# Performance work log

Measured on AMD Instinct MI355X. Metric: run time of the kernel, lower is better.

## Reference

```python
import jax, jax.numpy as jnp
import numpy as np

K = 10
EPS = 1e-5

def leaky(x):
    return jnp.where(x >= 0, x, 0.2 * x)

def graph_feature(x, k):
    # x: (B, C, N) -> edge features (B, 2C, N, k), standard DGCNN get_graph_feature
    B, C, N = x.shape
    xx = jnp.sum(x * x, axis=1)                      # (B, N)
    inner = jnp.einsum('bcn,bcm->bnm', x, x)          # (B, N, N)
    pair = 2.0 * inner - xx[:, :, None] - xx[:, None, :]  # -||xi - xj||^2
    _, idx = jax.lax.top_k(pair, k)                   # (B, N, k)
    xt = jnp.transpose(x, (0, 2, 1))                  # (B, N, C)
    nbr = xt[jnp.arange(B)[:, None, None], idx]       # (B, N, k, C) gather
    ctr = jnp.broadcast_to(xt[:, :, None, :], nbr.shape)
    feat = jnp.concatenate([nbr - ctr, ctr], axis=-1)  # (B, N, k, 2C)
    return jnp.transpose(feat, (0, 3, 1, 2))          # (B, 2C, N, k)

def edge_block(x, W, k):
    # gather -> 1x1 conv (edge MLP) -> leaky relu -> max over neighbors
    e = graph_feature(x, k)                           # (B, 2C, N, k)
    h = leaky(jnp.einsum('oc,bcnk->bonk', W, e))      # (B, O, N, k)
    return jnp.max(h, axis=-1)                        # (B, O, N)

def bn(x, g, b, m, v):
    # inference batchnorm over channel axis 1; x: (B, C, ...) 
    shape = (1, -1) + (1,) * (x.ndim - 2)
    return (x - m.reshape(shape)) * (g.reshape(shape) * jax.lax.rsqrt(v.reshape(shape) + EPS)) + b.reshape(shape)

def setup_inputs() -> dict:
    key = jax.random.key(0)
    ks = jax.random.split(key, 20)
    s = lambda i, shape, scale: (jax.random.normal(ks[i], shape, jnp.float32) * scale)
    inp = {
        'input': jax.random.normal(ks[0], (759, 220, 3), jnp.float32),
        'W1': s(1, (32, 6), 0.4),
        'W2': s(2, (32, 64), 0.15),
        'W3': s(3, (64, 64), 0.15),
        'W4': s(4, (128, 128), 0.1),
        'W5': s(5, (512, 256), 0.08),
        'g5': 1.0 + s(6, (512,), 0.05), 'b5': s(7, (512,), 0.05),
        'm5': s(8, (512,), 0.05), 'v5': 1.0 + 0.1 * jax.random.uniform(ks[9], (512,), jnp.float32),
        'Wl1': s(10, (1024, 1024), 0.03),
        'g6': 1.0 + s(11, (1024,), 0.05), 'b6': s(12, (1024,), 0.05),
        'm6': s(13, (1024,), 0.05), 'v6': 1.0 + 0.1 * jax.random.uniform(ks[14], (1024,), jnp.float32),
        'Wl2': s(15, (380, 1024), 0.03),
        'bl2': s(16, (380,), 0.02),
    }
    return inp

def reference(input, W1, W2, W3, W4, W5, g5, b5, m5, v5, Wl1, g6, b6, m6, v6, Wl2, bl2):
    x = jnp.transpose(input.reshape(-1, 220, 3), (0, 2, 1))  # (B, 3, N)
    x1 = edge_block(x, W1, K)    # (B, 32, N)
    x2 = edge_block(x1, W2, K)   # (B, 32, N)
    x3 = edge_block(x2, W3, K)   # (B, 64, N)
    x4 = edge_block(x3, W4, K)   # (B, 128, N)
    xc = jnp.concatenate([x1, x2, x3, x4], axis=1)           # (B, 256, N)
    h = leaky(bn(jnp.einsum('oc,bcn->bon', W5, xc), g5, b5, m5, v5))  # (B, 512, N)
    p = jnp.concatenate([jnp.max(h, axis=-1), jnp.mean(h, axis=-1)], axis=1)  # (B, 1024)
    z = leaky(bn(p @ Wl1.T, g6, b6, m6, v6))  # dropout is identity in eval
    return z @ Wl2.T + bl2                     # (B, 380)
```

## Files before the change

### kernel.cpp

```cpp
#include <hip/hip_runtime.h>
#include <math.h>

#define NB 759
#define NPT 220
#define KNN 10
#define XCCH 256
#define LDXC (XCCH * NPT)

typedef float f4 __attribute__((ext_vector_type(4)));
typedef float f16v __attribute__((ext_vector_type(16)));
typedef short bf8v __attribute__((ext_vector_type(8)));
typedef unsigned u4v __attribute__((ext_vector_type(4)));

__device__ inline unsigned short bfh(float x) {
  unsigned u = __float_as_uint(x);
  unsigned r = u + 0x7FFFu + ((u >> 16) & 1u);
  return (unsigned short)(r >> 16);
}
__device__ inline float bff(unsigned short h) {
  return __uint_as_float(((unsigned)h) << 16);
}
__device__ inline void bfsplit(float x, unsigned short& h, unsigned short& l) {
  h = bfh(x);
  l = bfh(x - bff(h));
}

__global__ __launch_bounds__(256) void k_transpose(const float* __restrict__ in, float* __restrict__ x0) {
  int i = blockIdx.x * 256 + threadIdx.x;
  if (i >= NB * 3 * NPT) return;
  int n = i % NPT; int t = i / NPT; int c = t % 3; int b = t / 3;
  x0[i] = in[(b * NPT + n) * 3 + c];
}

__global__ __launch_bounds__(256) void k_w5split(const float* __restrict__ W5,
    unsigned short* __restrict__ Wh, unsigned short* __restrict__ Wl) {
  int i = blockIdx.x * 256 + threadIdx.x;
  if (i >= 512 * 256) return;
  bfsplit(W5[i], Wh[i], Wl[i]);
}

__device__ inline void topk_insert(float d, int m, float* tv, int* ti) {
  if (d > tv[KNN - 1]) {
    tv[KNN - 1] = d; ti[KNN - 1] = m;
    #pragma unroll
    for (int j = KNN - 1; j >= 1; --j) {
      if (tv[j] > tv[j - 1]) {
        float tf = tv[j - 1]; tv[j - 1] = tv[j]; tv[j] = tf;
        int tq = ti[j - 1]; ti[j - 1] = ti[j]; ti[j] = tq;
      } else break;
    }
  }
}

__global__ __launch_bounds__(256) void k_knn3(const float* __restrict__ x, int ldb,
                                              int* __restrict__ idxout) {
  __shared__ __align__(16) float xl[NPT * 4];
  __shared__ float xx[NPT];
  int b = blockIdx.x;
  const float* xb = x + (size_t)b * ldb;
  for (int i = threadIdx.x; i < NPT; i += 256) {
    f4 v; v.x = xb[i]; v.y = xb[NPT + i]; v.z = xb[2 * NPT + i]; v.w = 0.f;
    *(f4*)&xl[i * 4] = v;
    xx[i] = v.x * v.x + v.y * v.y + v.z * v.z;
  }
  __syncthreads();
  int n = threadIdx.x;
  if (n >= NPT) return;
  f4 xn = *(const f4*)&xl[n * 4];
  float xxn = xx[n];
  float tv[KNN]; int ti[KNN];
  #pragma unroll
  for (int k = 0; k < KNN; ++k) { tv[k] = -1e30f; ti[k] = 0; }
  for (int m = 0; m < NPT; ++m) {
    f4 v = *(const f4*)&xl[m * 4];
    float dot = xn.x * v.x + xn.y * v.y + xn.z * v.z;
    topk_insert(2.f * dot - xxn - xx[m], m, tv, ti);
  }
  int* ib = idxout + ((size_t)b * NPT + n) * KNN;
  #pragma unroll
  for (int k = 0; k < KNN; ++k) ib[k] = ti[k];
}

template<int C>
__global__ __launch_bounds__(512) void k_knn_mfma(const float* __restrict__ x, int ldb,
                                                  int* __restrict__ idxout) {
  constexpr int KPG = C + 8;
  constexpr int SW = (C / 16) - 1;
  __shared__ __align__(16) unsigned short XH[224 * KPG];
  __shared__ __align__(16) unsigned short XM[224 * KPG];
  __shared__ __align__(16) unsigned short XL[224 * KPG];
  __shared__ float xx[224];
  int b = blockIdx.x;
  const float* xb = x + (size_t)b * ldb;
  for (int i = threadIdx.x; i < C * 224; i += 512) {
    int c = i / 224, m = i - c * 224;
    float v = (m < NPT) ? xb[c * NPT + m] : 0.f;
    unsigned short h = bfh(v);
    float r1 = v - bff(h);
    unsigned short mm = bfh(r1);
    unsigned short l = bfh(r1 - bff(mm));
    int cs = c ^ ((m & SW) << 4);
    XH[m * KPG + cs] = h; XM[m * KPG + cs] = mm; XL[m * KPG + cs] = l;
  }
  for (int m = threadIdx.x; m < 224; m += 512) {
    float s = 0.f;
    if (m < NPT) {
      for (int c = 0; c < C; ++c) { float v = xb[c * NPT + m]; s += v * v; }
    } else s = 1e30f;
    xx[m] = s;
  }
  __syncthreads();
  int w = threadIdx.x >> 6;
  int lane = threadIdx.x & 63;
  int lc = lane & 31, hi = lane >> 5;
  float tv[KNN]; int ti[KNN];
  #pragma unroll
  for (int k = 0; k < KNN; ++k) { tv[k] = -1e30f; ti[k] = 0; }
  if (w < 7) {
    int n = w * 32 + lc;
    f16v acc[7];
    #pragma unroll
    for (int mt = 0; mt < 7; ++mt)
      #pragma unroll
      for (int i = 0; i < 16; ++i) acc[mt][i] = 0.f;
    #pragma unroll
    for (int ks = 0; ks < C / 16; ++ks) {
      int kb = ks * 16 + hi * 8;
      int nsw = kb ^ ((n & SW) << 4);
      bf8v bh = *(const bf8v*)&XH[n * KPG + nsw];
      bf8v bm = *(const bf8v*)&XM[n * KPG + nsw];
      bf8v bl = *(const bf8v*)&XL[n * KPG + nsw];
      #pragma unroll
      for (int mt = 0; mt < 7; ++mt) {
        int mr = mt * 32 + lc;
        int msw = kb ^ ((mr & SW) << 4);
        bf8v ah = *(const bf8v*)&XH[mr * KPG + msw];
        bf8v am = *(const bf8v*)&XM[mr * KPG + msw];
        bf8v al = *(const bf8v*)&XL[mr * KPG + msw];
        acc[mt] = __builtin_amdgcn_mfma_f32_32x32x16_bf16(ah, bh, acc[mt], 0, 0, 0);
        acc[mt] = __builtin_amdgcn_mfma_f32_32x32x16_bf16(am, bh, acc[mt], 0, 0, 0);
        acc[mt] = __builtin_amdgcn_mfma_f32_32x32x16_bf16(ah, bm, acc[mt], 0, 0, 0);
        acc[mt] = __builtin_amdgcn_mfma_f32_32x32x16_bf16(am, bm, acc[mt], 0, 0, 0);
        acc[mt] = __builtin_amdgcn_mfma_f32_32x32x16_bf16(al, bh, acc[mt], 0, 0, 0);
        acc[mt] = __builtin_amdgcn_mfma_f32_32x32x16_bf16(ah, bl, acc[mt], 0, 0, 0);
      }
    }
    float xxn = xx[n];
    #pragma unroll
    for (int mt = 0; mt < 7; ++mt)
      #pragma unroll
      for (int i = 0; i < 16; ++i) {
        int m = mt * 32 + (i & 3) + 8 * (i >> 2) + 4 * hi;
        float d = 2.f * acc[mt][i] - xx[m] - xxn;
        topk_insert(d, m, tv, ti);
      }
  }
  __syncthreads();
  float* LV = (float*)XH;
  int* LI = (int*)XM;
  if (w < 7) {
    int slot = (w * 64 + lane) * KNN;
    #pragma unroll
    for (int k = 0; k < KNN; ++k) { LV[slot + k] = tv[k]; LI[slot + k] = ti[k]; }
  }
  __syncthreads();
  if (w < 7 && hi == 0) {
    int n = w * 32 + lc;
    if (n < NPT) {
      int sa = (w * 64 + lane) * KNN, sb = sa + 32 * KNN;
      int a = 0, bq = 0;
      int* ob = idxout + ((size_t)b * NPT + n) * KNN;
      #pragma unroll
      for (int k = 0; k < KNN; ++k) {
        float va = LV[sa + a], vb = LV[sb + bq];
        int ia = LI[sa + a], ic = LI[sb + bq];
        bool ta = (va > vb) || (va == vb && ia < ic);
        ob[k] = ta ? ia : ic;
        if (ta) ++a; else ++bq;
      }
    }
  }
}

template<int CIN, int OG, bool WBF16, bool WF32>
__global__ __launch_bounds__(512, 4) void k_conv_fused(const float* __restrict__ x, int ldb,
    const float* __restrict__ W, const int* __restrict__ idxb, float* __restrict__ xout, int ldo,
    unsigned short* __restrict__ xch, unsigned short* __restrict__ xcl, int cbase) {
  constexpr int NPAD = 224;
  constexpr int DBS = 224;
  constexpr int REGION = 64 * DBS;
  __shared__ __align__(16) float smem[REGION + CIN * 64];
  __shared__ unsigned short idxl[NPT * KNN];
  float* xl = smem;
  float* db = smem;
  float* wl = smem + REGION;
  int d = blockIdx.x;
  int b, og;
  if (OG == 4)      { b = (d & 7) * 95 + (d >> 5); og = (d >> 3) & 3; }
  else if (OG == 2) { b = (d & 7) * 95 + (d >> 4); og = (d >> 3) & 1; }
  else              { b = d; og = 0; }
  if (b >= NB) return;
  const float* xb = x + (size_t)b * ldb;
  for (int i = threadIdx.x; i < CIN * NPAD; i += 512) {
    int c = i / NPAD, n = i - c * NPAD;
    xl[i] = (n < NPT) ? xb[c * NPT + n] : 0.f;
  }
  for (int i = threadIdx.x; i < 64 * CIN; i += 512) {
    int rl = i & 63, c = i >> 6;
    int o = og * 32 + (rl & 31);
    float wv = (rl < 32) ? W[o * 2 * CIN + c]
                         : (W[o * 2 * CIN + CIN + c] - W[o * 2 * CIN + c]);
    wl[c * 64 + rl] = wv;
  }
  for (int i = threadIdx.x; i < NPT * KNN; i += 512)
    idxl[i] = (unsigned short)idxb[(size_t)b * NPT * KNN + i];
  __syncthreads();
  int rq = threadIdx.x & 15, nq = threadIdx.x >> 4;
  int gv[2]; bool gok[2];
  #pragma unroll
  for (int j = 0; j < 2; ++j) { int g = nq + j * 32; gok[j] = g < 55; gv[j] = (g < 55 ? g : 54) * 4; }
  f4 acc[2][4];
  #pragma unroll
  for (int j = 0; j < 2; ++j)
    #pragma unroll
    for (int i2 = 0; i2 < 4; ++i2) acc[j][i2] = (f4){0.f, 0.f, 0.f, 0.f};
  #pragma unroll 2
  for (int c = 0; c < CIN; ++c) {
    f4 wv = *(const f4*)&wl[c * 64 + rq * 4];
    #pragma unroll
    for (int j = 0; j < 2; ++j) {
      f4 xv = *(const f4*)&xl[c * NPAD + gv[j]];
      acc[j][0] += wv.x * xv; acc[j][1] += wv.y * xv;
      acc[j][2] += wv.z * xv; acc[j][3] += wv.w * xv;
    }
  }
  __syncthreads();
  #pragma unroll
  for (int j = 0; j < 2; ++j) {
    if (gok[j]) {
      #pragma unroll
      for (int i2 = 0; i2 < 4; ++i2)
        *(f4*)&db[(rq * 4 + i2) * DBS + gv[j]] = acc[j][i2];
    }
  }
  __syncthreads();
  int o0 = og * 32;
  for (int i = threadIdx.x; i < 32 * 224; i += 512) {
    int ol = i / 224, n = i - ol * 224;
    unsigned short h = 0, l = 0;
    if (n < NPT) {
      const float* drow = &db[ol * DBS];
      const unsigned short* ib = &idxl[n * KNN];
      float mx = -1e30f;
      #pragma unroll
      for (int k = 0; k < KNN; ++k) mx = fmaxf(mx, drow[ib[k]]);
      float v = mx + db[(32 + ol) * DBS + n];
      v = (v >= 0.f) ? v : 0.2f * v;
      if (WF32) xout[((size_t)b * ldo + o0 + ol) * NPT + n] = v;
      if (WBF16) bfsplit(v, h, l);
    }
    if (WBF16) {
      int c = cbase + o0 + ol;
      size_t off = (((size_t)b * 32 + (c >> 3)) * 224 + n) * 8 + (c & 7);
      xch[off] = h;
      xcl[off] = l;
    }
  }
}

__global__ __launch_bounds__(256) void k_w5_mfma_ps(
    const unsigned short* __restrict__ xch, const unsigned short* __restrict__ xcl,
    const unsigned short* __restrict__ Wh, const unsigned short* __restrict__ Wl,
    const float* __restrict__ g5, const float* __restrict__ b5, const float* __restrict__ m5,
    const float* __restrict__ v5, float* __restrict__ p) {
  __shared__ __align__(16) unsigned short XH[4 * 224 * 8];
  __shared__ __align__(16) unsigned short XL[4 * 224 * 8];
  int d = blockIdx.x;
  int b = (d & 7) * 95 + (d >> 5);
  int rg = (d >> 3) & 3;
  if (b >= NB) return;
  int lane = threadIdx.x & 63, w = threadIdx.x >> 6;
  f16v acc[7];
  #pragma unroll
  for (int t = 0; t < 7; ++t)
    #pragma unroll
    for (int i = 0; i < 16; ++i) acc[t][i] = 0.f;

  int r = rg * 128 + w * 32 + (lane & 31);
  int khalf = (lane >> 5) * 8;
  const u4v* srcH = (const u4v*)(xch + (size_t)b * 57344);
  const u4v* srcL = (const u4v*)(xcl + (size_t)b * 57344);
  u4v* dH = (u4v*)XH;
  u4v* dL = (u4v*)XL;

  for (int cb = 0; cb < 8; ++cb) {
    if (cb) __syncthreads();
    const u4v* sH = srcH + cb * 896;
    const u4v* sL = srcL + cb * 896;
    for (int i = threadIdx.x; i < 896; i += 256) {
      dH[i] = sH[i];
      dL[i] = sL[i];
    }
    __syncthreads();
    #pragma unroll
    for (int ks = 0; ks < 2; ++ks) {
      int kg = cb * 32 + ks * 16 + khalf;
      int g = ks * 2 + (lane >> 5);
      bf8v ah = *(const bf8v*)&Wh[(size_t)r * 256 + kg];
      bf8v al = *(const bf8v*)&Wl[(size_t)r * 256 + kg];
      #pragma unroll
      for (int t = 0; t < 7; ++t) {
        int col = t * 32 + (lane & 31);
        bf8v bh = *(const bf8v*)&XH[g * 1792 + col * 8];
        bf8v bl = *(const bf8v*)&XL[g * 1792 + col * 8];
        acc[t] = __builtin_amdgcn_mfma_f32_32x32x16_bf16(ah, bh, acc[t], 0, 0, 0);
        acc[t] = __builtin_amdgcn_mfma_f32_32x32x16_bf16(al, bh, acc[t], 0, 0, 0);
        acc[t] = __builtin_amdgcn_mfma_f32_32x32x16_bf16(ah, bl, acc[t], 0, 0, 0);
      }
    }
  }
  int rbase = rg * 128 + w * 32 + 4 * (lane >> 5);
  int lc = lane & 31;
  #pragma unroll
  for (int i = 0; i < 16; ++i) {
    int row = rbase + (i & 3) + 8 * (i >> 2);
    float a = g5[row] * rsqrtf(v5[row] + 1e-5f);
    float dq = b5[row] - m5[row] * a;
    float mx = -1e30f, sm = 0.f;
    #pragma unroll
    for (int t = 0; t < 7; ++t) {
      bool valid = (t < 6) || (lc < 28);
      float hv = a * acc[t][i] + dq;
      float lv = (hv >= 0.f) ? hv : 0.2f * hv;
      if (valid) { mx = fmaxf(mx, lv); sm += lv; }
    }
    #pragma unroll
    for (int m_ = 1; m_ <= 16; m_ <<= 1) {
      mx = fmaxf(mx, __shfl_xor(mx, m_));
      sm += __shfl_xor(sm, m_);
    }
    if (lc == 0) {
      p[(size_t)b * 1024 + row] = mx;
      p[(size_t)b * 1024 + 512 + row] = sm * (1.f / NPT);
    }
  }
}

#define KP 72
__global__ __launch_bounds__(256) void k_w5_mfma(const float* __restrict__ xc,
    const unsigned short* __restrict__ Wh, const unsigned short* __restrict__ Wl,
    const float* __restrict__ g5, const float* __restrict__ b5, const float* __restrict__ m5,
    const float* __restrict__ v5, float* __restrict__ p) {
  __shared__ __align__(16) unsigned short XH[224 * KP];
  __shared__ __align__(16) unsigned short XL[224 * KP];
  int d = blockIdx.x;
  int b = (d & 7) * 95 + (d >> 5);
  int rg = (d >> 3) & 3;
  if (b >= NB) return;
  int lane = threadIdx.x & 63, w = threadIdx.x >> 6;
  f16v acc[7];
  #pragma unroll
  for (int t = 0; t < 7; ++t)
    #pragma unroll
    for (int i = 0; i < 16; ++i) acc[t][i] = 0.f;

  int r = rg * 128 + w * 32 + (lane & 31);
  int khalf = (lane >> 5) * 8;

  for (int cb = 0; cb < 4; ++cb) {
    if (cb) __syncthreads();
    for (int i = threadIdx.x; i < 32 * NPT; i += 256) {
      int cp = i / NPT;
      int n = i - cp * NPT;
      int c0 = cp * 2;
      const float* src = &xc[((size_t)b * XCCH + cb * 64 + c0) * NPT + n];
      float x0 = src[0];
      float x1 = src[NPT];
      unsigned short h0, l0, h1, l1;
      bfsplit(x0, h0, l0); bfsplit(x1, h1, l1);
      ((unsigned*)XH)[(n * KP + c0) >> 1] = (unsigned)h0 | ((unsigned)h1 << 16);
      ((unsigned*)XL)[(n * KP + c0) >> 1] = (unsigned)l0 | ((unsigned)l1 << 16);
    }
    for (int i = threadIdx.x; i < 4 * 32; i += 256) {
      int n = NPT + (i >> 5); int cd = i & 31;
      ((unsigned*)XH)[n * (KP / 2) + cd] = 0u;
      ((unsigned*)XL)[n * (KP / 2) + cd] = 0u;
    }
    __syncthreads();
    #pragma unroll
    for (int ks = 0; ks < 4; ++ks) {
      int kg = cb * 64 + ks * 16 + khalf;
      int kl = ks * 16 + khalf;
      bf8v ah = *(const bf8v*)&Wh[(size_t)r * 256 + kg];
      bf8v al = *(const bf8v*)&Wl[(size_t)r * 256 + kg];
      #pragma unroll
      for (int t = 0; t < 7; ++t) {
        int col = t * 32 + (lane & 31);
        bf8v bh = *(const bf8v*)&XH[col * KP + kl];
        bf8v bl = *(const bf8v*)&XL[col * KP + kl];
        acc[t] = __builtin_amdgcn_mfma_f32_32x32x16_bf16(ah, bh, acc[t], 0, 0, 0);
        acc[t] = __builtin_amdgcn_mfma_f32_32x32x16_bf16(al, bh, acc[t], 0, 0, 0);
        acc[t] = __builtin_amdgcn_mfma_f32_32x32x16_bf16(ah, bl, acc[t], 0, 0, 0);
      }
    }
  }
  int rbase = rg * 128 + w * 32 + 4 * (lane >> 5);
  int lc = lane & 31;
  #pragma unroll
  for (int i = 0; i < 16; ++i) {
    int row = rbase + (i & 3) + 8 * (i >> 2);
    float a = g5[row] * rsqrtf(v5[row] + 1e-5f);
    float dq = b5[row] - m5[row] * a;
    float mx = -1e30f, sm = 0.f;
    #pragma unroll
    for (int t = 0; t < 7; ++t) {
      bool valid = (t < 6) || (lc < 28);
      float hv = a * acc[t][i] + dq;
      float lv = (hv >= 0.f) ? hv : 0.2f * hv;
      if (valid) { mx = fmaxf(mx, lv); sm += lv; }
    }
    #pragma unroll
    for (int m_ = 1; m_ <= 16; m_ <<= 1) {
      mx = fmaxf(mx, __shfl_xor(mx, m_));
      sm += __shfl_xor(sm, m_);
    }
    if (lc == 0) {
      p[(size_t)b * 1024 + row] = mx;
      p[(size_t)b * 1024 + 512 + row] = sm * (1.f / NPT);
    }
  }
}

template<int ON, bool FUSE>
__global__ __launch_bounds__(256) void k_fc(const float* __restrict__ in, const float* __restrict__ Wt,
    const float* __restrict__ q0, const float* __restrict__ q1, const float* __restrict__ q2,
    const float* __restrict__ q3, float* __restrict__ out, int ostride) {
  __shared__ __align__(16) float il[32 * 68];
  __shared__ __align__(16) float wl[32 * 68];
  int b0 = blockIdx.x * 64, o0 = blockIdx.y * 64;
  int oq = threadIdx.x & 15, bq = threadIdx.x >> 4;
  f4 acc[4];
  #pragma unroll
  for (int i2 = 0; i2 < 4; ++i2) acc[i2] = (f4){0.f, 0.f, 0.f, 0.f};
  for (int cb = 0; cb < 32; ++cb) {
    if (cb) __syncthreads();
    for (int i = threadIdx.x; i < 2048; i += 256) {
      int c = i & 31, bb = i >> 5;
      il[c * 68 + bb] = (b0 + bb < NB) ? in[(b0 + bb) * 1024 + cb * 32 + c] : 0.f;
    }
    for (int i = threadIdx.x; i < 2048; i += 256) {
      int c = i & 31, ol = i >> 5;
      wl[c * 68 + ol] = (o0 + ol < ON) ? Wt[(o0 + ol) * 1024 + cb * 32 + c] : 0.f;
    }
    __syncthreads();
    #pragma unroll
    for (int c = 0; c < 32; ++c) {
      f4 wv = *(const f4*)&wl[c * 68 + oq * 4];
      f4 iv = *(const f4*)&il[c * 68 + bq * 4];
      acc[0] += wv.x * iv; acc[1] += wv.y * iv; acc[2] += wv.z * iv; acc[3] += wv.w * iv;
    }
  }
  #pragma unroll
  for (int i2 = 0; i2 < 4; ++i2) {
    int o = o0 + oq * 4 + i2;
    if (o >= ON) continue;
    float A = 1.f, Dv = 0.f;
    if (FUSE) { float a = q0[o] * rsqrtf(q3[o] + 1e-5f); A = a; Dv = q1[o] - q2[o] * a; }
    else { Dv = q0[o]; }
    #pragma unroll
    for (int jj = 0; jj < 4; ++jj) {
      int bb = b0 + bq * 4 + jj;
      if (bb < NB) {
        float v = acc[i2][jj];
        if (FUSE) { v = A * v + Dv; v = (v >= 0.f) ? v : 0.2f * v; }
        else { v = v + Dv; }
        out[(size_t)bb * ostride + o] = v;
      }
    }
  }
}

extern "C" void kernel_launch(void* const* d_in, const int* in_sizes, int n_in,
                              void* d_out, int out_size, void* d_ws, size_t ws_size,
                              hipStream_t stream) {
  const float* input = (const float*)d_in[0];
  const float* W1 = (const float*)d_in[1];
  const float* W2 = (const float*)d_in[2];
  const float* W3 = (const float*)d_in[3];
  const float* W4 = (const float*)d_in[4];
  const float* W5 = (const float*)d_in[5];
  const float* g5 = (const float*)d_in[6];
  const float* b5 = (const float*)d_in[7];
  const float* m5 = (const float*)d_in[8];
  const float* v5 = (const float*)d_in[9];
  const float* Wl1 = (const float*)d_in[10];
  const float* g6 = (const float*)d_in[11];
  const float* b6 = (const float*)d_in[12];
  const float* m6 = (const float*)d_in[13];
  const float* v6 = (const float*)d_in[14];
  const float* Wl2 = (const float*)d_in[15];
  const float* bl2 = (const float*)d_in[16];

  float* w = (float*)d_ws;
  bool ps = ws_size >= 276000000ull;

  float *x0, *xc, *p, *z; int* idxb;
  unsigned short *wh, *wlo, *xch, *xcl;
  int ldxc, ldo;
  if (ps) {
    x0 = w;
    xc = x0 + 500940;
    p  = xc + 21373440;
    z  = p  + 777216;
    idxb = (int*)(z + 777216);
    wh  = (unsigned short*)(w + 25098612);
    wlo = wh + 131072;
    xch = wlo + 131072;
    xcl = xch + 43524096;
    ldxc = 128 * NPT; ldo = 128;
  } else {
    x0 = w;
    xc = x0 + 500940;
    p  = xc + 42746880;
    z  = p  + 777216;
    idxb = (int*)(z + 777216);
    wh  = (unsigned short*)(w + 46472052);
    wlo = wh + 131072;
    xch = wlo; xcl = wlo;
    ldxc = LDXC; ldo = XCCH;
  }

  k_transpose<<<1957, 256, 0, stream>>>(input, x0);
  k_w5split<<<512, 256, 0, stream>>>(W5, wh, wlo);

  k_knn3<<<759, 256, 0, stream>>>(x0, 3 * NPT, idxb);

  if (ps) {
    k_conv_fused<3, 1, true, true><<<759, 512, 0, stream>>>(x0, 3 * NPT, W1, idxb, xc, ldo, xch, xcl, 0);
    k_knn_mfma<32><<<759, 512, 0, stream>>>(xc, ldxc, idxb);
    k_conv_fused<32, 1, true, true><<<759, 512, 0, stream>>>(xc, ldxc, W2, idxb, xc + 32 * NPT, ldo, xch, xcl, 32);
    k_knn_mfma<32><<<759, 512, 0, stream>>>(xc + 32 * NPT, ldxc, idxb);
    k_conv_fused<32, 2, true, true><<<1520, 512, 0, stream>>>(xc + 32 * NPT, ldxc, W3, idxb, xc + 64 * NPT, ldo, xch, xcl, 64);
    k_knn_mfma<64><<<759, 512, 0, stream>>>(xc + 64 * NPT, ldxc, idxb);
    k_conv_fused<64, 4, true, false><<<3040, 512, 0, stream>>>(xc + 64 * NPT, ldxc, W4, idxb, xc, 0, xch, xcl, 128);
    k_w5_mfma_ps<<<3040, 256, 0, stream>>>(xch, xcl, wh, wlo, g5, b5, m5, v5, p);
  } else {
    k_conv_fused<3, 1, false, true><<<759, 512, 0, stream>>>(x0, 3 * NPT, W1, idxb, xc, ldo, xch, xcl, 0);
    k_knn_mfma<32><<<759, 512, 0, stream>>>(xc, ldxc, idxb);
    k_conv_fused<32, 1, false, true><<<759, 512, 0, stream>>>(xc, ldxc, W2, idxb, xc + 32 * NPT, ldo, xch, xcl, 32);
    k_knn_mfma<32><<<759, 512, 0, stream>>>(xc + 32 * NPT, ldxc, idxb);
    k_conv_fused<32, 2, false, true><<<1520, 512, 0, stream>>>(xc + 32 * NPT, ldxc, W3, idxb, xc + 64 * NPT, ldo, xch, xcl, 64);
    k_knn_mfma<64><<<759, 512, 0, stream>>>(xc + 64 * NPT, ldxc, idxb);
    k_conv_fused<64, 4, false, true><<<3040, 512, 0, stream>>>(xc + 64 * NPT, ldxc, W4, idxb, xc + 128 * NPT, ldo, xch, xcl, 128);
    k_w5_mfma<<<3040, 256, 0, stream>>>(xc, wh, wlo, g5, b5, m5, v5, p);
  }

  k_fc<1024, true><<<dim3(12, 16), 256, 0, stream>>>(p, Wl1, g6, b6, m6, v6, z, 1024);
  k_fc<380, false><<<dim3(12, 6), 256, 0, stream>>>(z, Wl2, bl2, bl2, bl2, bl2, (float*)d_out, 380);
}
```

Before: 1.581 ms.

## Pre-split only upper xc channels to bf16 hi/lo, convert lower channels in W5 kernel

Drops the separate full pre-split path, in which every conv wrote bf16 hi/lo copies of all 256 concat channels. Now only the top 64*NCH channels (chosen by available workspace) are written pre-split, in a padded KP=72 layout matching the W5 kernel's shared-memory tile. The W5 MFMA kernel converts the lower channel blocks from fp32 on the fly and copies the upper blocks directly. This removes split writes from early layers and unifies the two W5 kernels, at the cost of a bit more padding traffic and a branchier loader.

```diff
diff --git a/kernel.cpp b/kernel.cpp
--- a/kernel.cpp
+++ b/kernel.cpp
@@ -6,6 +6,7 @@
 #define KNN 10
 #define XCCH 256
 #define LDXC (XCCH * NPT)
+#define KP 72
 
 typedef float f4 __attribute__((ext_vector_type(4)));
 typedef float f16v __attribute__((ext_vector_type(16)));
@@ -185,7 +186,8 @@
 template<int CIN, int OG, bool WBF16, bool WF32>
 __global__ __launch_bounds__(512, 4) void k_conv_fused(const float* __restrict__ x, int ldb,
     const float* __restrict__ W, const int* __restrict__ idxb, float* __restrict__ xout, int ldo,
-    unsigned short* __restrict__ xch, unsigned short* __restrict__ xcl, int cbase) {
+    unsigned short* __restrict__ xch, unsigned short* __restrict__ xcl, int cbase,
+    int csplit, int nch) {
   constexpr int NPAD = 224;
   constexpr int DBS = 224;
   constexpr int REGION = 64 * DBS;
@@ -261,93 +263,19 @@
     }
     if (WBF16) {
       int c = cbase + o0 + ol;
-      size_t off = (((size_t)b * 32 + (c >> 3)) * 224 + n) * 8 + (c & 7);
-      xch[off] = h;
-      xcl[off] = l;
-    }
-  }
-}
-
-__global__ __launch_bounds__(256) void k_w5_mfma_ps(
-    const unsigned short* __restrict__ xch, const unsigned short* __restrict__ xcl,
-    const unsigned short* __restrict__ Wh, const unsigned short* __restrict__ Wl,
-    const float* __restrict__ g5, const float* __restrict__ b5, const float* __restrict__ m5,
-    const float* __restrict__ v5, float* __restrict__ p) {
-  __shared__ __align__(16) unsigned short XH[4 * 224 * 8];
-  __shared__ __align__(16) unsigned short XL[4 * 224 * 8];
-  int d = blockIdx.x;
-  int b = (d & 7) * 95 + (d >> 5);
-  int rg = (d >> 3) & 3;
-  if (b >= NB) return;
-  int lane = threadIdx.x & 63, w = threadIdx.x >> 6;
-  f16v acc[7];
-  #pragma unroll
-  for (int t = 0; t < 7; ++t)
-    #pragma unroll
-    for (int i = 0; i < 16; ++i) acc[t][i] = 0.f;
-
-  int r = rg * 128 + w * 32 + (lane & 31);
-  int khalf = (lane >> 5) * 8;
-  const u4v* srcH = (const u4v*)(xch + (size_t)b * 57344);
-  const u4v* srcL = (const u4v*)(xcl + (size_t)b * 57344);
-  u4v* dH = (u4v*)XH;
-  u4v* dL = (u4v*)XL;
-
-  for (int cb = 0; cb < 8; ++cb) {
-    if (cb) __syncthreads();
-    const u4v* sH = srcH + cb * 896;
-    const u4v* sL = srcL + cb * 896;
-    for (int i = threadIdx.x; i < 896; i += 256) {
-      dH[i] = sH[i];
-      dL[i] = sL[i];
-    }
-    __syncthreads();
-    #pragma unroll
-    for (int ks = 0; ks < 2; ++ks) {
-      int kg = cb * 32 + ks * 16 + khalf;
-      int g = ks * 2 + (lane >> 5);
-      bf8v ah = *(const bf8v*)&Wh[(size_t)r * 256 + kg];
-      bf8v al = *(const bf8v*)&Wl[(size_t)r * 256 + kg];
-      #pragma unroll
-      for (int t = 0; t < 7; ++t) {
-        int col = t * 32 + (lane & 31);
-        bf8v bh = *(const bf8v*)&XH[g * 1792 + col * 8];
-        bf8v bl = *(const bf8v*)&XL[g * 1792 + col * 8];
-        acc[t] = __builtin_amdgcn_mfma_f32_32x32x16_bf16(ah, bh, acc[t], 0, 0, 0);
-        acc[t] = __builtin_amdgcn_mfma_f32_32x32x16_bf16(al, bh, acc[t], 0, 0, 0);
-        acc[t] = __builtin_amdgcn_mfma_f32_32x32x16_bf16(ah, bl, acc[t], 0, 0, 0);
-      }
-    }
-  }
-  int rbase = rg * 128 + w * 32 + 4 * (lane >> 5);
-  int lc = lane & 31;
-  #pragma unroll
-  for (int i = 0; i < 16; ++i) {
-    int row = rbase + (i & 3) + 8 * (i >> 2);
-    float a = g5[row] * rsqrtf(v5[row] + 1e-5f);
-    float dq = b5[row] - m5[row] * a;
-    float mx = -1e30f, sm = 0.f;
-    #pragma unroll
-    for (int t = 0; t < 7; ++t) {
-      bool valid = (t < 6) || (lc < 28);
-      float hv = a * acc[t][i] + dq;
-      float lv = (hv >= 0.f) ? hv : 0.2f * hv;
-      if (valid) { mx = fmaxf(mx, lv); sm += lv; }
-    }
-    #pragma unroll
-    for (int m_ = 1; m_ <= 16; m_ <<= 1) {
-      mx = fmaxf(mx, __shfl_xor(mx, m_));
-      sm += __shfl_xor(sm, m_);
-    }
-    if (lc == 0) {
-      p[(size_t)b * 1024 + row] = mx;
-      p[(size_t)b * 1024 + 512 + row] = sm * (1.f / NPT);
-    }
-  }
-}
-
-#define KP 72
-__global__ __launch_bounds__(256) void k_w5_mfma(const float* __restrict__ xc,
+      if (c >= csplit) {
+        int cc = c - csplit;
+        size_t off = (((size_t)b * nch + (cc >> 6)) * 224 + n) * (size_t)KP + (cc & 63);
+        xch[off] = h;
+        xcl[off] = l;
+      }
+    }
+  }
+}
+
+__global__ __launch_bounds__(256) void k_w5_mfma(const float* __restrict__ xc, int chs,
+    const unsigned short* __restrict__ xh, const unsigned short* __restrict__ xlo,
+    int split_cb, int nch,
     const unsigned short* __restrict__ Wh, const unsigned short* __restrict__ Wl,
     const float* __restrict__ g5, const float* __restrict__ b5, const float* __restrict__ m5,
     const float* __restrict__ v5, float* __restrict__ p) {
@@ -369,22 +297,34 @@
 
   for (int cb = 0; cb < 4; ++cb) {
     if (cb) __syncthreads();
-    for (int i = threadIdx.x; i < 32 * NPT; i += 256) {
-      int cp = i / NPT;
-      int n = i - cp * NPT;
-      int c0 = cp * 2;
-      const float* src = &xc[((size_t)b * XCCH + cb * 64 + c0) * NPT + n];
-      float x0 = src[0];
-      float x1 = src[NPT];
-      unsigned short h0, l0, h1, l1;
-      bfsplit(x0, h0, l0); bfsplit(x1, h1, l1);
-      ((unsigned*)XH)[(n * KP + c0) >> 1] = (unsigned)h0 | ((unsigned)h1 << 16);
-      ((unsigned*)XL)[(n * KP + c0) >> 1] = (unsigned)l0 | ((unsigned)l1 << 16);
-    }
-    for (int i = threadIdx.x; i < 4 * 32; i += 256) {
-      int n = NPT + (i >> 5); int cd = i & 31;
-      ((unsigned*)XH)[n * (KP / 2) + cd] = 0u;
-      ((unsigned*)XL)[n * (KP / 2) + cd] = 0u;
+    if (cb < split_cb) {
+      for (int i = threadIdx.x; i < 32 * NPT; i += 256) {
+        int cp = i / NPT;
+        int n = i - cp * NPT;
+        int c0 = cp * 2;
+        const float* src = &xc[((size_t)b * chs + cb * 64 + c0) * NPT + n];
+        float x0 = src[0];
+        float x1 = src[NPT];
+        unsigned short h0, l0, h1, l1;
+        bfsplit(x0, h0, l0); bfsplit(x1, h1, l1);
+        ((unsigned*)XH)[(n * KP + c0) >> 1] = (unsigned)h0 | ((unsigned)h1 << 16);
+        ((unsigned*)XL)[(n * KP + c0) >> 1] = (unsigned)l0 | ((unsigned)l1 << 16);
+      }
+      for (int i = threadIdx.x; i < 4 * 32; i += 256) {
+        int n = NPT + (i >> 5); int cd = i & 31;
+        ((unsigned*)XH)[n * (KP / 2) + cd] = 0u;
+        ((unsigned*)XL)[n * (KP / 2) + cd] = 0u;
+      }
+    } else {
+      int q = cb - split_cb;
+      const u4v* sH = (const u4v*)(xh + (((size_t)b * nch + q) * 224) * KP);
+      const u4v* sL = (const u4v*)(xlo + (((size_t)b * nch + q) * 224) * KP);
+      u4v* dH = (u4v*)XH;
+      u4v* dL = (u4v*)XL;
+      for (int i = threadIdx.x; i < 224 * KP / 8; i += 256) {
+        dH[i] = sH[i];
+        dL[i] = sL[i];
+      }
     }
     __syncthreads();
     #pragma unroll
@@ -502,12 +442,14 @@
   const float* bl2 = (const float*)d_in[16];
 
   float* w = (float*)d_ws;
-  bool ps = ws_size >= 276000000ull;
+  int NCH = 0;
+  if (ws_size >= 4ull * (25229684ull + 12241152ull * 3)) NCH = 3;
+  else if (ws_size >= 4ull * (25229684ull + 12241152ull * 2)) NCH = 2;
 
   float *x0, *xc, *p, *z; int* idxb;
-  unsigned short *wh, *wlo, *xch, *xcl;
-  int ldxc, ldo;
-  if (ps) {
+  unsigned short *wh, *wlo, *xh, *xlo;
+  int chs, csplit, split_cb;
+  if (NCH > 0) {
     x0 = w;
     xc = x0 + 500940;
     p  = xc + 21373440;
@@ -515,9 +457,9 @@
     idxb = (int*)(z + 777216);
     wh  = (unsigned short*)(w + 25098612);
     wlo = wh + 131072;
-    xch = wlo + 131072;
-    xcl = xch + 43524096;
-    ldxc = 128 * NPT; ldo = 128;
+    xh  = wlo + 131072;
+    xlo = xh + (size_t)NCH * 12241152;
+    chs = 128; csplit = 256 - 64 * NCH; split_cb = 4 - NCH;
   } else {
     x0 = w;
     xc = x0 + 500940;
@@ -526,34 +468,43 @@
     idxb = (int*)(z + 777216);
     wh  = (unsigned short*)(w + 46472052);
     wlo = wh + 131072;
-    xch = wlo; xcl = wlo;
-    ldxc = LDXC; ldo = XCCH;
-  }
+    xh = wlo; xlo = wlo;
+    chs = 256; csplit = 256; split_cb = 4;
+  }
+  int ldxc = chs * NPT;
 
   k_transpose<<<1957, 256, 0, stream>>>(input, x0);
   k_w5split<<<512, 256, 0, stream>>>(W5, wh, wlo);
 
   k_knn3<<<759, 256, 0, stream>>>(x0, 3 * NPT, idxb);
 
-  if (ps) {
-    k_conv_fused<3, 1, true, true><<<759, 512, 0, stream>>>(x0, 3 * NPT, W1, idxb, xc, ldo, xch, xcl, 0);
+  if (NCH == 3) {
+    k_conv_fused<3, 1, false, true><<<759, 512, 0, stream>>>(x0, 3 * NPT, W1, idxb, xc, chs, xh, xlo, 0, csplit, NCH);
     k_knn_mfma<32><<<759, 512, 0, stream>>>(xc, ldxc, idxb);
-    k_conv_fused<32, 1, true, true><<<759, 512, 0, stream>>>(xc, ldxc, W2, idxb, xc + 32 * NPT, ldo, xch, xcl, 32);
+    k_conv_fused<32, 1, false, true><<<759, 512, 0, stream>>>(xc, ldxc, W2, idxb, xc + 32 * NPT, chs, xh, xlo, 32, csplit, NCH);
     k_knn_mfma<32><<<759, 512, 0, stream>>>(xc + 32 * NPT, ldxc, idxb);
-    k_conv_fused<32, 2, true, true><<<1520, 512, 0, stream>>>(xc + 32 * NPT, ldxc, W3, idxb, xc + 64 * NPT, ldo, xch, xcl, 64);
+    k_conv_fused<32, 2, true, true><<<1520, 512, 0, stream>>>(xc + 32 * NPT, ldxc, W3, idxb, xc + 64 * NPT, chs, xh, xlo, 64, csplit, NCH);
     k_knn_mfma<64><<<759, 512, 0, stream>>>(xc + 64 * NPT, ldxc, idxb);
-    k_conv_fused<64, 4, true, false><<<3040, 512, 0, stream>>>(xc + 64 * NPT, ldxc, W4, idxb, xc, 0, xch, xcl, 128);
-    k_w5_mfma_ps<<<3040, 256, 0, stream>>>(xch, xcl, wh, wlo, g5, b5, m5, v5, p);
+    k_conv_fused<64, 4, true, false><<<3040, 512, 0, stream>>>(xc + 64 * NPT, ldxc, W4, idxb, xc, 0, xh, xlo, 128, csplit, NCH);
+  } else if (NCH == 2) {
+    k_conv_fused<3, 1, false, true><<<759, 512, 0, stream>>>(x0, 3 * NPT, W1, idxb, xc, chs, xh, xlo, 0, csplit, NCH);
+    k_knn_mfma<32><<<759, 512, 0, stream>>>(xc, ldxc, idxb);
+    k_conv_fused<32, 1, false, true><<<759, 512, 0, stream>>>(xc, ldxc, W2, idxb, xc + 32 * NPT, chs, xh, xlo, 32, csplit, NCH);
+    k_knn_mfma<32><<<759, 512, 0, stream>>>(xc + 32 * NPT, ldxc, idxb);
+    k_conv_fused<32, 2, false, true><<<1520, 512, 0, stream>>>(xc + 32 * NPT, ldxc, W3, idxb, xc + 64 * NPT, chs, xh, xlo, 64, csplit, NCH);
+    k_knn_mfma<64><<<759, 512, 0, stream>>>(xc + 64 * NPT, ldxc, idxb);
+    k_conv_fused<64, 4, true, false><<<3040, 512, 0, stream>>>(xc + 64 * NPT, ldxc, W4, idxb, xc, 0, xh, xlo, 128, csplit, NCH);
   } else {
-    k_conv_fused<3, 1, false, true><<<759, 512, 0, stream>>>(x0, 3 * NPT, W1, idxb, xc, ldo, xch, xcl, 0);
+    k_conv_fused<3, 1, false, true><<<759, 512, 0, stream>>>(x0, 3 * NPT, W1, idxb, xc, chs, xh, xlo, 0, csplit, NCH);
     k_knn_mfma<32><<<759, 512, 0, stream>>>(xc, ldxc, idxb);
-    k_conv_fused<32, 1, false, true><<<759, 512, 0, stream>>>(xc, ldxc, W2, idxb, xc + 32 * NPT, ldo, xch, xcl, 32);
+    k_conv_fused<32, 1, false, true><<<759, 512, 0, stream>>>(xc, ldxc, W2, idxb, xc + 32 * NPT, chs, xh, xlo, 32, csplit, NCH);
     k_knn_mfma<32><<<759, 512, 0, stream>>>(xc + 32 * NPT, ldxc, idxb);
-    k_conv_fused<32, 2, false, true><<<1520, 512, 0, stream>>>(xc + 32 * NPT, ldxc, W3, idxb, xc + 64 * NPT, ldo, xch, xcl, 64);
+    k_conv_fused<32, 2, false, true><<<1520, 512, 0, stream>>>(xc + 32 * NPT, ldxc, W3, idxb, xc + 64 * NPT, chs, xh, xlo, 64, csplit, NCH);
     k_knn_mfma<64><<<759, 512, 0, stream>>>(xc + 64 * NPT, ldxc, idxb);
-    k_conv_fused<64, 4, false, true><<<3040, 512, 0, stream>>>(xc + 64 * NPT, ldxc, W4, idxb, xc + 128 * NPT, ldo, xch, xcl, 128);
-    k_w5_mfma<<<3040, 256, 0, stream>>>(xc, wh, wlo, g5, b5, m5, v5, p);
-  }
+    k_conv_fused<64, 4, false, true><<<3040, 512, 0, stream>>>(xc + 64 * NPT, ldxc, W4, idxb, xc + 128 * NPT, chs, xh, xlo, 128, csplit, NCH);
+  }
+
+  k_w5_mfma<<<3040, 256, 0, stream>>>(xc, chs, xh, xlo, split_cb, NCH, wh, wlo, g5, b5, m5, v5, p);
 
   k_fc<1024, true><<<dim3(12, 16), 256, 0, stream>>>(p, Wl1, g6, b6, m6, v6, z, 1024);
   k_fc<380, false><<<dim3(12, 6), 256, 0, stream>>>(z, Wl2, bl2, bl2, bl2, bl2, (float*)d_out, 380);
```

After: 1.712 ms. +8.3%, slower.
